# Performance work log

Measured on AMD Instinct MI355X. Metric: run time of the kernel, lower is better.

Reference implementation:

```python
import jax, jax.numpy as jnp
import numpy as np

N_NODES = 50000


def sage_conv(x, src, dst, Wl, bl, Wr, n_nodes):
    # PyG SAGEConv (aggr='mean', root_weight=True, bias on lin_l):
    #   out = lin_l(mean_{j in N(i)} x_j) + lin_r(x_i)
    msg = x[src]  # [E, d] gather
    s = jax.ops.segment_sum(msg, dst, num_segments=n_nodes)  # [N, d]
    cnt = jax.ops.segment_sum(jnp.ones((src.shape[0], 1), x.dtype), dst,
                              num_segments=n_nodes)  # [N, 1]
    agg = s / jnp.maximum(cnt, 1.0)
    return agg @ Wl.T + bl + x @ Wr.T


def setup_inputs() -> dict:
    key = jax.random.key(0)
    ks = jax.random.split(key, 8)
    in_c, hid_c, out_c = 256, 256, 2
    x = jax.random.normal(ks[0], (N_NODES, in_c), dtype=jnp.float32)
    edge_index = jax.random.randint(ks[1], (2, 800000), 0, N_NODES, dtype=jnp.int64)
    def lin(k, fan_out, fan_in):
        bound = 1.0 / np.sqrt(fan_in)
        return jax.random.uniform(k, (fan_out, fan_in), jnp.float32, -bound, bound)
    return {
        "x": x,
        "edge_index": edge_index,
        "W1l": lin(ks[2], hid_c, in_c),
        "b1": jnp.zeros((hid_c,), jnp.float32),
        "W1r": lin(ks[3], hid_c, in_c),
        "W2l": lin(ks[4], out_c, hid_c),
        "b2": jnp.zeros((out_c,), jnp.float32),
        "W2r": lin(ks[5], out_c, hid_c),
    }


def reference(x, edge_index, W1l, b1, W1r, W2l, b2, W2r):
    src, dst = edge_index[0], edge_index[1]
    h = sage_conv(x, src, dst, W1l, b1, W1r, N_NODES)
    h = jax.nn.relu(h)
    # dropout is identity in eval mode (training=False)
    out = sage_conv(h, src, dst, W2l, b2, W2r, N_NODES)
    return jax.nn.log_softmax(out, axis=1)
```

## Files before the change

kernel.cpp:

```cpp
#include <hip/hip_runtime.h>
#include <math.h>

#define DIM 256
#define GBM 128
#define GBN 128
#define GBK 64
#define SCHUNK 1024

typedef short bf16x8 __attribute__((ext_vector_type(8)));
typedef float f32x4 __attribute__((ext_vector_type(4)));

__device__ __forceinline__ ushort f2bf(float f) {
  uint u = __float_as_uint(f);
  u += 0x7fffu + ((u >> 16) & 1u);
  return (ushort)(u >> 16);
}
__device__ __forceinline__ float bf2f(uint bits) {
  return __uint_as_float(bits << 16);
}

__device__ __forceinline__ void async_copy16(const ushort* g, ushort* l) {
  __builtin_amdgcn_global_load_lds(
      (const __attribute__((address_space(1))) unsigned int*)g,
      (__attribute__((address_space(3))) unsigned int*)l, 16, 0, 0);
}

__global__ __launch_bounds__(256) void prep_kernel(
    const float4* __restrict__ x4, ushort* __restrict__ xb, int n4,
    const float* __restrict__ Wl, const float* __restrict__ Wr,
    const float* __restrict__ W2l, const float* __restrict__ W2r,
    ushort* __restrict__ Wb, ushort* __restrict__ W2b,
    const int* __restrict__ dst, int* __restrict__ deg, int E) {
  const int t0 = blockIdx.x * blockDim.x + threadIdx.x;
  const int stride = gridDim.x * blockDim.x;
  for (int i = t0; i < n4; i += stride) {
    const float4 v = x4[i];
    ushort4 o;
    o.x = f2bf(v.x); o.y = f2bf(v.y); o.z = f2bf(v.z); o.w = f2bf(v.w);
    *(ushort4*)&xb[i * 4] = o;
  }
  if (t0 < 131072) {
    const int n = t0 >> 9, k = t0 & 511;
    const float v = (k < 256) ? Wl[n * 256 + k] : Wr[n * 256 + (k - 256)];
    Wb[t0] = f2bf(v);
  } else if (t0 < 135168) {
    const int w2 = t0 - 131072;
    const int row = w2 >> 8, k = w2 & 255;
    float v = 0.f;
    if (row < 2)      v = W2l[row * 256 + k];
    else if (row < 4) v = W2r[(row - 2) * 256 + k];
    W2b[w2] = f2bf(v);
  }
  for (int e = t0; e < E; e += stride) atomicAdd(&deg[dst[e]], 1);
}

__global__ __launch_bounds__(256) void scan_partial(
    const int* __restrict__ deg, int* __restrict__ bsum, int M) {
  const int base = blockIdx.x * SCHUNK + threadIdx.x * 4;
  int s = 0;
  if (base + 3 < M) {
    const int4 v = *(const int4*)(deg + base);
    s = v.x + v.y + v.z + v.w;
  } else {
    for (int j = 0; j < 4; ++j) if (base + j < M) s += deg[base + j];
  }
  #pragma unroll
  for (int off = 32; off; off >>= 1) s += __shfl_xor(s, off);
  __shared__ int ws[4];
  if ((threadIdx.x & 63) == 0) ws[threadIdx.x >> 6] = s;
  __syncthreads();
  if (threadIdx.x == 0) bsum[blockIdx.x] = ws[0] + ws[1] + ws[2] + ws[3];
}

__global__ __launch_bounds__(1024) void scan_sums(
    int* __restrict__ bsum, int nb) {
  __shared__ int sh[1024];
  const int t = threadIdx.x;
  const int orig = (t < nb) ? bsum[t] : 0;
  sh[t] = orig;
  __syncthreads();
  for (int off = 1; off < 1024; off <<= 1) {
    const int v = sh[t];
    const int u = (t >= off) ? sh[t - off] : 0;
    __syncthreads();
    sh[t] = v + u;
    __syncthreads();
  }
  if (t < nb) bsum[t] = sh[t] - orig;
}

__global__ __launch_bounds__(256) void scan_finalize(
    const int* __restrict__ deg, const int* __restrict__ bsum,
    int* __restrict__ rowptr, int* __restrict__ fill,
    float* __restrict__ invc, int M) {
  const int t = threadIdx.x;
  const int lane = t & 63;
  const int wid = t >> 6;
  const int base = blockIdx.x * SCHUNK + t * 4;
  int d[4];
  #pragma unroll
  for (int j = 0; j < 4; ++j) d[j] = (base + j < M) ? deg[base + j] : 0;
  const int tsum = d[0] + d[1] + d[2] + d[3];
  int v = tsum;
  #pragma unroll
  for (int off = 1; off < 64; off <<= 1) {
    const int u = __shfl_up(v, off);
    if (lane >= off) v += u;
  }
  __shared__ int wtot[4];
  if (lane == 63) wtot[wid] = v;
  __syncthreads();
  int wbase = 0;
  for (int w = 0; w < wid; ++w) wbase += wtot[w];
  int run = bsum[blockIdx.x] + wbase + v - tsum;
  #pragma unroll
  for (int j = 0; j < 4; ++j) {
    const int idx = base + j;
    if (idx < M) {
      rowptr[idx] = run;
      fill[idx]   = run;
      invc[idx]   = 1.0f / fmaxf((float)d[j], 1.0f);
      run += d[j];
      if (idx == M - 1) rowptr[M] = run;
    }
  }
}

__global__ __launch_bounds__(256) void scatter_edges(
    const int* __restrict__ src, const int* __restrict__ dst,
    int* __restrict__ fill, int* __restrict__ esrc, int E) {
  int e = blockIdx.x * blockDim.x + threadIdx.x;
  if (e < E) {
    const int pos = atomicAdd(&fill[dst[e]], 1);
    esrc[pos] = src[e];
  }
}

__global__ __launch_bounds__(256) void gather1(
    const ushort* __restrict__ xb, const int* __restrict__ esrc,
    const int* __restrict__ rowptr, const float* __restrict__ invc,
    ushort* __restrict__ aggb, int M) {
  const int lane = threadIdx.x & 63;
  const int wave = threadIdx.x >> 6;
  const int half = lane >> 5;
  const int fl   = lane & 31;
  const int i = blockIdx.x * 4 + wave;
  if (i >= M) return;
  const int k0 = rowptr[i];
  const int k1 = rowptr[i + 1];
  float s0 = 0.f, s1 = 0.f, s2 = 0.f, s3 = 0.f;
  float s4 = 0.f, s5 = 0.f, s6 = 0.f, s7 = 0.f;

#define ACC(v)                                                  \
  do {                                                          \
    s0 += bf2f((v).x & 0xffffu); s1 += bf2f((v).x >> 16);       \
    s2 += bf2f((v).y & 0xffffu); s3 += bf2f((v).y >> 16);       \
    s4 += bf2f((v).z & 0xffffu); s5 += bf2f((v).z >> 16);       \
    s6 += bf2f((v).w & 0xffffu); s7 += bf2f((v).w >> 16);       \
  } while (0)

  int k = k0;
  for (; k + 7 < k1; k += 8) {
    const int e0 = esrc[k + 0 + half];
    const int e1 = esrc[k + 2 + half];
    const int e2 = esrc[k + 4 + half];
    const int e3 = esrc[k + 6 + half];
    const uint4 v0 = *(const uint4*)(xb + (size_t)e0 * DIM + fl * 8);
    const uint4 v1 = *(const uint4*)(xb + (size_t)e1 * DIM + fl * 8);
    const uint4 v2 = *(const uint4*)(xb + (size_t)e2 * DIM + fl * 8);
    const uint4 v3 = *(const uint4*)(xb + (size_t)e3 * DIM + fl * 8);
    ACC(v0); ACC(v1); ACC(v2); ACC(v3);
  }
  for (; k + 1 < k1; k += 2) {
    const int e = esrc[k + half];
    const uint4 v = *(const uint4*)(xb + (size_t)e * DIM + fl * 8);
    ACC(v);
  }
  if (k < k1 && half == 0) {
    const uint4 v = *(const uint4*)(xb + (size_t)esrc[k] * DIM + fl * 8);
    ACC(v);
  }
#undef ACC

  s0 += __shfl_xor(s0, 32); s1 += __shfl_xor(s1, 32);
  s2 += __shfl_xor(s2, 32); s3 += __shfl_xor(s3, 32);
  s4 += __shfl_xor(s4, 32); s5 += __shfl_xor(s5, 32);
  s6 += __shfl_xor(s6, 32); s7 += __shfl_xor(s7, 32);

  if (half == 0) {
    const float inv = invc[i];
    uint4 o;
    o.x = (uint)f2bf(s0 * inv) | ((uint)f2bf(s1 * inv) << 16);
    o.y = (uint)f2bf(s2 * inv) | ((uint)f2bf(s3 * inv) << 16);
    o.z = (uint)f2bf(s4 * inv) | ((uint)f2bf(s5 * inv) << 16);
    o.w = (uint)f2bf(s6 * inv) | ((uint)f2bf(s7 * inv) << 16);
    *(uint4*)(aggb + (size_t)i * DIM + fl * 8) = o;
  }
}

__global__ __launch_bounds__(256) void gemm1_mfma(
    const ushort* __restrict__ Ab, const ushort* __restrict__ Xb,
    const ushort* __restrict__ Wb, const float* __restrict__ b1,
    ushort* __restrict__ Hb, int M) {
  __shared__ __align__(16) ushort lds[2 * GBM * GBK];
  ushort* As = lds;
  ushort* Bs = lds + GBM * GBK;

  const int tid  = threadIdx.x;
  const int lane = tid & 63;
  const int wave = tid >> 6;
  const int wm = wave >> 1, wn = wave & 1;
  const int row0 = blockIdx.x * GBM;
  const int col0 = blockIdx.y * GBN;

  const int lsub = lane >> 3;
  const int lk   = lane & 7;

  const int frow = lane & 15;
  const int fk   = (lane >> 4) * 8;

  f32x4 acc[4][4] = {};

  for (int t = 0; t < 8; ++t) {
    const int kt = t * GBK;
    const ushort* srcA = (t < 4) ? Ab : Xb;
    const int kofs = kt & 255;
    #pragma unroll
    for (int i = 0; i < 4; ++i) {
      const int rbase = i * 32 + wave * 8;
      const int r = rbase + lsub;
      async_copy16(srcA + (size_t)(row0 + r) * DIM + kofs + lk * 8,
                   &As[rbase * GBK]);
      async_copy16(Wb + (size_t)(col0 + r) * 512 + kt + lk * 8,
                   &Bs[rbase * GBK]);
    }
    __syncthreads();

    #pragma unroll
    for (int s = 0; s < 2; ++s) {
      bf16x8 a[4], b[4];
      #pragma unroll
      for (int i = 0; i < 4; ++i)
        a[i] = *(const bf16x8*)&As[(wm * 64 + i * 16 + frow) * GBK + s * 32 + fk];
      #pragma unroll
      for (int j = 0; j < 4; ++j)
        b[j] = *(const bf16x8*)&Bs[(wn * 64 + j * 16 + frow) * GBK + s * 32 + fk];
      #pragma unroll
      for (int i = 0; i < 4; ++i)
        #pragma unroll
        for (int j = 0; j < 4; ++j)
          acc[i][j] = __builtin_amdgcn_mfma_f32_16x16x32_bf16(a[i], b[j], acc[i][j], 0, 0, 0);
    }
    __syncthreads();
  }

  #pragma unroll
  for (int i = 0; i < 4; ++i) {
    #pragma unroll
    for (int j = 0; j < 4; ++j) {
      const int col = wn * 64 + j * 16 + frow;
      const float bias = b1[col0 + col];
      #pragma unroll
      for (int r = 0; r < 4; ++r) {
        const int row = wm * 64 + i * 16 + (lane >> 4) * 4 + r;
        lds[row * 128 + (col ^ ((row & 7) << 3))] =
            f2bf(fmaxf(acc[i][j][r] + bias, 0.f));
      }
    }
  }
  __syncthreads();
  for (int c = tid; c < 128 * 16; c += 256) {
    const int row = c >> 4;
    const int grow = row0 + row;
    if (grow < M) {
      const uint4 v = *(const uint4*)&lds[row * 128 + (((c & 15) ^ (row & 7)) * 8)];
      *(uint4*)(Hb + (size_t)grow * DIM + col0 + (c & 15) * 8) = v;
    }
  }
}

__global__ __launch_bounds__(256) void proj2_mfma(
    const ushort* __restrict__ Hb, const ushort* __restrict__ W2b,
    float* __restrict__ Y4v, int M) {
  const int lane = threadIdx.x & 63;
  const int wave = threadIdx.x >> 6;
  const int row0 = (blockIdx.x * 4 + wave) * 16;
  if (row0 >= M) return;
  const int frow = lane & 15;
  const int fk   = (lane >> 4) * 8;

  f32x4 acc = {};
  #pragma unroll
  for (int s = 0; s < 8; ++s) {
    bf16x8 a = {};
    if (row0 + frow < M)
      a = *(const bf16x8*)(Hb + (size_t)(row0 + frow) * DIM + s * 32 + fk);
    const bf16x8 b = *(const bf16x8*)(W2b + frow * DIM + s * 32 + fk);
    acc = __builtin_amdgcn_mfma_f32_16x16x32_bf16(a, b, acc, 0, 0, 0);
  }
  const int col = lane & 15;
  if (col < 4) {
    #pragma unroll
    for (int r = 0; r < 4; ++r) {
      const int row = row0 + (lane >> 4) * 4 + r;
      if (row < M) Y4v[(size_t)row * 4 + col] = acc[r];
    }
  }
}

__global__ __launch_bounds__(256) void layer2_finalize(
    const float2* __restrict__ Y2, const int* __restrict__ esrc,
    const int* __restrict__ rowptr, const float* __restrict__ invc,
    const float* __restrict__ b2, float* __restrict__ out, int M) {
  int i = blockIdx.x * blockDim.x + threadIdx.x;
  if (i < M) {
    const int k0 = rowptr[i];
    const int k1 = rowptr[i + 1];
    float a0 = 0.f, a1 = 0.f;
    int k = k0;
    for (; k + 3 < k1; k += 4) {
      const int e0 = esrc[k], e1 = esrc[k + 1], e2 = esrc[k + 2], e3 = esrc[k + 3];
      const float2 y0 = Y2[2 * (size_t)e0];
      const float2 y1 = Y2[2 * (size_t)e1];
      const float2 y2 = Y2[2 * (size_t)e2];
      const float2 y3 = Y2[2 * (size_t)e3];
      a0 += y0.x + y1.x + y2.x + y3.x;
      a1 += y0.y + y1.y + y2.y + y3.y;
    }
    for (; k < k1; ++k) {
      const float2 y = Y2[2 * (size_t)esrc[k]];
      a0 += y.x; a1 += y.y;
    }
    const float inv = invc[i];
    const float2 yr = Y2[2 * (size_t)i + 1];
    const float o0 = a0 * inv + yr.x + b2[0];
    const float o1 = a1 * inv + yr.y + b2[1];
    const float m = fmaxf(o0, o1);
    const float lse = m + logf(expf(o0 - m) + expf(o1 - m));
    out[2 * i + 0] = o0 - lse;
    out[2 * i + 1] = o1 - lse;
  }
}

extern "C" void kernel_launch(void* const* d_in, const int* in_sizes, int n_in,
                              void* d_out, int out_size, void* d_ws, size_t ws_size,
                              hipStream_t stream) {
  const float* x   = (const float*)d_in[0];
  const int*   ei  = (const int*)d_in[1];
  const float* W1l = (const float*)d_in[2];
  const float* b1  = (const float*)d_in[3];
  const float* W1r = (const float*)d_in[4];
  const float* W2l = (const float*)d_in[5];
  const float* b2  = (const float*)d_in[6];
  const float* W2r = (const float*)d_in[7];

  const int E = in_sizes[1] / 2;
  const int M = in_sizes[0] / DIM;
  const int* src = ei;
  const int* dst = ei + E;

  char* ws = (char*)d_ws;
  size_t off = 0;
  ushort* xb   = (ushort*)(ws + off); off += (size_t)M * DIM * 2;
  ushort* aggb = (ushort*)(ws + off); off += (size_t)M * DIM * 2;
  ushort* Hb   = (ushort*)(ws + off); off += (size_t)M * DIM * 2;
  ushort* Wb   = (ushort*)(ws + off); off += (size_t)256 * 512 * 2;
  ushort* W2b  = (ushort*)(ws + off); off += (size_t)16 * 256 * 2;
  float* Y4v   = (float*)(ws + off);  off += (size_t)M * 4 * 4;
  float* invc  = (float*)(ws + off);  off += (size_t)M * 4;
  int* deg     = (int*)(ws + off);    off += (size_t)M * 4;
  int* fill    = (int*)(ws + off);    off += (size_t)M * 4;
  int* rowptr  = (int*)(ws + off);    off += (size_t)(M + 1) * 4;
  int* bsum    = (int*)(ws + off);    off += 1024 * 4;
  int* esrc    = (int*)(ws + off);    off += (size_t)E * 4;

  hipMemsetAsync(deg, 0, (size_t)M * 4, stream);

  const int EB = (E + 255) / 256;
  const int NB = (M + SCHUNK - 1) / SCHUNK;

  prep_kernel<<<2048, 256, 0, stream>>>((const float4*)x, xb, M * DIM / 4,
                                        W1l, W1r, W2l, W2r, Wb, W2b, dst, deg, E);
  scan_partial<<<NB, 256, 0, stream>>>(deg, bsum, M);
  scan_sums<<<1, 1024, 0, stream>>>(bsum, NB);
  scan_finalize<<<NB, 256, 0, stream>>>(deg, bsum, rowptr, fill, invc, M);
  scatter_edges<<<EB, 256, 0, stream>>>(src, dst, fill, esrc, E);
  gather1<<<(M + 3) / 4, 256, 0, stream>>>(xb, esrc, rowptr, invc, aggb, M);

  dim3 g1((M + GBM - 1) / GBM, DIM / GBN);
  gemm1_mfma<<<g1, 256, 0, stream>>>(aggb, xb, Wb, b1, Hb, M);

  proj2_mfma<<<(M / 16 + 3) / 4 + 1, 256, 0, stream>>>(Hb, W2b, Y4v, M);
  layer2_finalize<<<(M + 255) / 256, 256, 0, stream>>>(
      (const float2*)Y4v, esrc, rowptr, invc, b2, (float*)d_out, M);
}
```

Measured before the change: 284.6 us.

## Fuse layer-2 projection into GEMM1 epilogue and software-pipeline gather loads

The layer-2 projection (H @ W2) now runs inside the GEMM1 epilogue from the relu'd tile already in LDS. Each 128-column block computes a partial product with MFMA and atomically adds it into Y4v, so the 25 MB bf16 H buffer is no longer written and read back and one kernel launch is removed. Y4v is zeroed together with deg in a single memset. Separately, gather1 double-buffers its row loads so the next batch of edge rows is in flight while the previous batch is accumulated. The cost is float atomics from two column blocks per row, which make the summation order nondeterministic, plus higher register pressure in gather.

```diff
diff --git a/kernel.cpp b/kernel.cpp
--- a/kernel.cpp
+++ b/kernel.cpp
@@ -151,6 +151,7 @@
   float s0 = 0.f, s1 = 0.f, s2 = 0.f, s3 = 0.f;
   float s4 = 0.f, s5 = 0.f, s6 = 0.f, s7 = 0.f;
 
+#define ROW(e) (*(const uint4*)(xb + (size_t)(e) * DIM + fl * 8))
 #define ACC(v)                                                  \
   do {                                                          \
     s0 += bf2f((v).x & 0xffffu); s1 += bf2f((v).x >> 16);       \
@@ -160,27 +161,37 @@
   } while (0)
 
   int k = k0;
-  for (; k + 7 < k1; k += 8) {
-    const int e0 = esrc[k + 0 + half];
-    const int e1 = esrc[k + 2 + half];
-    const int e2 = esrc[k + 4 + half];
-    const int e3 = esrc[k + 6 + half];
-    const uint4 v0 = *(const uint4*)(xb + (size_t)e0 * DIM + fl * 8);
-    const uint4 v1 = *(const uint4*)(xb + (size_t)e1 * DIM + fl * 8);
-    const uint4 v2 = *(const uint4*)(xb + (size_t)e2 * DIM + fl * 8);
-    const uint4 v3 = *(const uint4*)(xb + (size_t)e3 * DIM + fl * 8);
-    ACC(v0); ACC(v1); ACC(v2); ACC(v3);
+  if (k1 - k0 >= 16) {
+    uint4 a0 = ROW(esrc[k + 0 + half]);
+    uint4 a1 = ROW(esrc[k + 2 + half]);
+    uint4 a2 = ROW(esrc[k + 4 + half]);
+    uint4 a3 = ROW(esrc[k + 6 + half]);
+    k += 8;
+    for (; k + 7 < k1; k += 8) {
+      const uint4 b0 = ROW(esrc[k + 0 + half]);
+      const uint4 b1 = ROW(esrc[k + 2 + half]);
+      const uint4 b2 = ROW(esrc[k + 4 + half]);
+      const uint4 b3 = ROW(esrc[k + 6 + half]);
+      ACC(a0); ACC(a1); ACC(a2); ACC(a3);
+      a0 = b0; a1 = b1; a2 = b2; a3 = b3;
+    }
+    ACC(a0); ACC(a1); ACC(a2); ACC(a3);
+  }
+  for (; k + 3 < k1; k += 4) {
+    const uint4 v0 = ROW(esrc[k + 0 + half]);
+    const uint4 v1 = ROW(esrc[k + 2 + half]);
+    ACC(v0); ACC(v1);
   }
   for (; k + 1 < k1; k += 2) {
-    const int e = esrc[k + half];
-    const uint4 v = *(const uint4*)(xb + (size_t)e * DIM + fl * 8);
+    const uint4 v = ROW(esrc[k + half]);
     ACC(v);
   }
   if (k < k1 && half == 0) {
-    const uint4 v = *(const uint4*)(xb + (size_t)esrc[k] * DIM + fl * 8);
+    const uint4 v = ROW(esrc[k]);
     ACC(v);
   }
 #undef ACC
+#undef ROW
 
   s0 += __shfl_xor(s0, 32); s1 += __shfl_xor(s1, 32);
   s2 += __shfl_xor(s2, 32); s3 += __shfl_xor(s3, 32);
@@ -201,7 +212,7 @@
 __global__ __launch_bounds__(256) void gemm1_mfma(
     const ushort* __restrict__ Ab, const ushort* __restrict__ Xb,
     const ushort* __restrict__ Wb, const float* __restrict__ b1,
-    ushort* __restrict__ Hb, int M) {
+    const ushort* __restrict__ W2b, float* __restrict__ Y4v, int M) {
   __shared__ __align__(16) ushort lds[2 * GBM * GBK];
   ushort* As = lds;
   ushort* Bs = lds + GBM * GBK;
@@ -269,41 +280,30 @@
     }
   }
   __syncthreads();
-  for (int c = tid; c < 128 * 16; c += 256) {
-    const int row = c >> 4;
-    const int grow = row0 + row;
-    if (grow < M) {
-      const uint4 v = *(const uint4*)&lds[row * 128 + (((c & 15) ^ (row & 7)) * 8)];
-      *(uint4*)(Hb + (size_t)grow * DIM + col0 + (c & 15) * 8) = v;
-    }
-  }
-}
-
-__global__ __launch_bounds__(256) void proj2_mfma(
-    const ushort* __restrict__ Hb, const ushort* __restrict__ W2b,
-    float* __restrict__ Y4v, int M) {
-  const int lane = threadIdx.x & 63;
-  const int wave = threadIdx.x >> 6;
-  const int row0 = (blockIdx.x * 4 + wave) * 16;
-  if (row0 >= M) return;
-  const int frow = lane & 15;
-  const int fk   = (lane >> 4) * 8;
-
-  f32x4 acc = {};
-  #pragma unroll
-  for (int s = 0; s < 8; ++s) {
-    bf16x8 a = {};
-    if (row0 + frow < M)
-      a = *(const bf16x8*)(Hb + (size_t)(row0 + frow) * DIM + s * 32 + fk);
-    const bf16x8 b = *(const bf16x8*)(W2b + frow * DIM + s * 32 + fk);
-    acc = __builtin_amdgcn_mfma_f32_16x16x32_bf16(a, b, acc, 0, 0, 0);
-  }
-  const int col = lane & 15;
-  if (col < 4) {
+
+  bf16x8 wfrag[4];
+  #pragma unroll
+  for (int s2 = 0; s2 < 4; ++s2)
+    wfrag[s2] = *(const bf16x8*)(W2b + frow * DIM + col0 + s2 * 32 + fk);
+
+  #pragma unroll
+  for (int g = 0; g < 2; ++g) {
+    const int grp = wave * 2 + g;
+    f32x4 y = {};
     #pragma unroll
-    for (int r = 0; r < 4; ++r) {
-      const int row = row0 + (lane >> 4) * 4 + r;
-      if (row < M) Y4v[(size_t)row * 4 + col] = acc[r];
+    for (int s2 = 0; s2 < 4; ++s2) {
+      const int row = grp * 16 + frow;
+      const bf16x8 a =
+          *(const bf16x8*)&lds[row * 128 + ((s2 * 32 + fk) ^ ((row & 7) << 3))];
+      y = __builtin_amdgcn_mfma_f32_16x16x32_bf16(a, wfrag[s2], y, 0, 0, 0);
+    }
+    const int c = lane & 15;
+    if (c < 4) {
+      #pragma unroll
+      for (int r = 0; r < 4; ++r) {
+        const int grow = row0 + grp * 16 + (lane >> 4) * 4 + r;
+        if (grow < M) unsafeAtomicAdd(&Y4v[(size_t)grow * 4 + c], y[r]);
+      }
     }
   }
 }
@@ -361,20 +361,20 @@
 
   char* ws = (char*)d_ws;
   size_t off = 0;
+  float* Y4v  = (float*)(ws + off);  off += (size_t)M * 4 * 4;
+  int* deg    = (int*)(ws + off);    off += (size_t)M * 4;
+  const size_t zbytes = off;
   ushort* xb   = (ushort*)(ws + off); off += (size_t)M * DIM * 2;
   ushort* aggb = (ushort*)(ws + off); off += (size_t)M * DIM * 2;
-  ushort* Hb   = (ushort*)(ws + off); off += (size_t)M * DIM * 2;
   ushort* Wb   = (ushort*)(ws + off); off += (size_t)256 * 512 * 2;
   ushort* W2b  = (ushort*)(ws + off); off += (size_t)16 * 256 * 2;
-  float* Y4v   = (float*)(ws + off);  off += (size_t)M * 4 * 4;
   float* invc  = (float*)(ws + off);  off += (size_t)M * 4;
-  int* deg     = (int*)(ws + off);    off += (size_t)M * 4;
   int* fill    = (int*)(ws + off);    off += (size_t)M * 4;
   int* rowptr  = (int*)(ws + off);    off += (size_t)(M + 1) * 4;
   int* bsum    = (int*)(ws + off);    off += 1024 * 4;
   int* esrc    = (int*)(ws + off);    off += (size_t)E * 4;
 
-  hipMemsetAsync(deg, 0, (size_t)M * 4, stream);
+  hipMemsetAsync(d_ws, 0, zbytes, stream);
 
   const int EB = (E + 255) / 256;
   const int NB = (M + SCHUNK - 1) / SCHUNK;
@@ -388,9 +388,8 @@
   gather1<<<(M + 3) / 4, 256, 0, stream>>>(xb, esrc, rowptr, invc, aggb, M);
 
   dim3 g1((M + GBM - 1) / GBM, DIM / GBN);
-  gemm1_mfma<<<g1, 256, 0, stream>>>(aggb, xb, Wb, b1, Hb, M);
-
-  proj2_mfma<<<(M / 16 + 3) / 4 + 1, 256, 0, stream>>>(Hb, W2b, Y4v, M);
+  gemm1_mfma<<<g1, 256, 0, stream>>>(aggb, xb, Wb, b1, W2b, Y4v, M);
+
   layer2_finalize<<<(M + 255) / 256, 256, 0, stream>>>(
       (const float2*)Y4v, esrc, rowptr, invc, b2, (float*)d_out, M);
 }
```

Result: slower. 291.2 us (+2.3%).
